# Kernel tuning notes

Hardware: AMD Instinct MI355X
Metric: run time of the kernel (lower is better)

Reference implementation:

```python
import jax, jax.numpy as jnp
import numpy as np

H = 16  # num_attention_heads

def setup_inputs() -> dict:
    key = jax.random.key(0)
    ks = jax.random.split(key, 4)
    B, S, D = 4, 2048, 1024
    scale = 1.0 / np.sqrt(D)
    return {
        "hidden_states": jax.random.normal(ks[0], (B, S, D), dtype=jnp.float32),
        "attention_mask": jnp.zeros((B, 1, 1, S), dtype=jnp.float32),
        "Wq": jax.random.normal(ks[1], (D, D), dtype=jnp.float32) * scale,
        "bq": jnp.zeros((D,), dtype=jnp.float32),
        "Wk": jax.random.normal(ks[2], (D, D), dtype=jnp.float32) * scale,
        "bk": jnp.zeros((D,), dtype=jnp.float32),
        "Wv": jax.random.normal(ks[3], (D, D), dtype=jnp.float32) * scale,
        "bv": jnp.zeros((D,), dtype=jnp.float32),
    }

def _split_heads(x, B, S):
    # [B,S,D] -> [B,H,S,Dh]
    return x.reshape(B, S, H, -1).transpose(0, 2, 1, 3)

def reference(hidden_states, attention_mask, Wq, bq, Wk, bk, Wv, bv):
    B, S, D = hidden_states.shape
    Dh = D // H
    q = _split_heads(hidden_states @ Wq.T + bq, B, S)  # [B,H,S,Dh]
    k = _split_heads(hidden_states @ Wk.T + bk, B, S)
    v = _split_heads(hidden_states @ Wv.T + bv, B, S)
    scores = jnp.einsum("bhqd,bhkd->bhqk", q, k) / jnp.sqrt(jnp.float32(Dh))
    scores = scores + attention_mask  # additive mask, broadcast [B,1,1,S]
    probs = jax.nn.softmax(scores, axis=-1)  # dropout is identity in eval mode
    ctx = jnp.einsum("bhqk,bhkd->bhqd", probs, v)  # [B,H,S,Dh]
    ctx = ctx.transpose(0, 2, 1, 3).reshape(B, S, D)
    return ctx
```

## Files before the change

kernel.cpp:

```cpp
#include <hip/hip_runtime.h>
#include <hip/hip_bf16.h>
#include <stdint.h>

#define LOG2E 1.44269504088896340736f
#define SCL   (0.125f * LOG2E)

typedef __attribute__((ext_vector_type(8)))  short short8;
typedef __attribute__((ext_vector_type(4)))  float floatx4;
typedef __attribute__((ext_vector_type(16))) float floatx16;
typedef __attribute__((ext_vector_type(4)))  unsigned short ushort4v;

#define GLP(g, l)                                                              \
    __builtin_amdgcn_global_load_lds(                                          \
        (const __attribute__((address_space(1))) void*)(g),                    \
        (__attribute__((address_space(3))) void*)(l), 16, 0, 0)

#if __has_builtin(__builtin_amdgcn_exp2f)
#define EXP2(x) __builtin_amdgcn_exp2f(x)
#else
#define EXP2(x) exp2f(x)
#endif

static __device__ __forceinline__ unsigned short f2bf(float f) {
    union { float f; unsigned u; } v; v.f = f;
    unsigned r = v.u + 0x7FFFu + ((v.u >> 16) & 1u);
    return (unsigned short)(r >> 16);
}

static __device__ __forceinline__ unsigned pack2bf(float a, float b) {
    __hip_bfloat162 h = __float22bfloat162_rn(make_float2(a, b));
    union { __hip_bfloat162 h; unsigned u; } c; c.h = h; return c.u;
}

__global__ __launch_bounds__(256) void cvt_kernel(const float* __restrict__ in,
                                                  unsigned short* __restrict__ out,
                                                  int n4) {
    int i = blockIdx.x * 256 + threadIdx.x;
    if (i < n4) {
        float4 v = ((const float4*)in)[i];
        ushort4v o;
        o.x = f2bf(v.x); o.y = f2bf(v.y); o.z = f2bf(v.z); o.w = f2bf(v.w);
        ((ushort4v*)out)[i] = o;
    }
}

__global__ __launch_bounds__(256) void cvt_w3m(const float* __restrict__ Wq,
                                               const float* __restrict__ Wk,
                                               const float* __restrict__ Wv,
                                               const float* __restrict__ mask,
                                               unsigned short* __restrict__ out,
                                               float* __restrict__ maskl) {
    int i = blockIdx.x * 256 + threadIdx.x;
    if (i < 786432) {
        const float* src; int j;
        if (i < 262144)      { src = Wq; j = i; }
        else if (i < 524288) { src = Wk; j = i - 262144; }
        else                 { src = Wv; j = i - 524288; }
        float4 v = ((const float4*)src)[j];
        ushort4v o;
        o.x = f2bf(v.x); o.y = f2bf(v.y); o.z = f2bf(v.z); o.w = f2bf(v.w);
        ((ushort4v*)out)[i] = o;
    } else if (i < 786432 + 2048) {
        int j = i - 786432;
        float4 v = ((const float4*)mask)[j];
        ((float4*)maskl)[j] = make_float4(v.x * LOG2E, v.y * LOG2E,
                                          v.z * LOG2E, v.w * LOG2E);
    }
}

__global__ __launch_bounds__(256) void qkv_gemm(
        const unsigned short* __restrict__ X,
        const unsigned short* __restrict__ W,
        const float* __restrict__ bq, const float* __restrict__ bk,
        const float* __restrict__ bv,
        unsigned short* __restrict__ Qf,
        unsigned short* __restrict__ Kf,
        unsigned short* __restrict__ Vt)
{
    __shared__ __align__(16) unsigned short sh[17408];
    unsigned short* Ash = sh;
    unsigned short* Bsh = sh + 8192;

    const int tid  = threadIdx.x;
    const int lane = tid & 63;
    const int wv   = tid >> 6;
    const int quad = lane >> 4;
    const int ln   = lane & 15;
    const int mBase = blockIdx.x * 128;
    const int nBase = blockIdx.y * 128;
    const int wm = (wv >> 1) * 64;
    const int wn = (wv & 1) * 64;

    floatx4 acc[4][4];
#pragma unroll
    for (int i = 0; i < 4; ++i)
#pragma unroll
        for (int j = 0; j < 4; ++j) acc[i][j] = 0.0f;

    const int sr = lane >> 3;
    const int kc = (lane & 7) ^ sr;

    for (int kb = 0; kb < 1024; kb += 64) {
        __syncthreads();
#pragma unroll
        for (int s = 0; s < 4; ++s) {
            const int seg = wv * 4 + s;
            const int row = seg * 8 + sr;
            GLP(X + (size_t)(mBase + row) * 1024 + kb + kc * 8, Ash + seg * 512);
            GLP(W + (size_t)(nBase + row) * 1024 + kb + kc * 8, Bsh + seg * 512);
        }
        __syncthreads();
#pragma unroll
        for (int kk = 0; kk < 2; ++kk) {
            const int c = kk * 4 + quad;
            short8 aF[4], bF[4];
#pragma unroll
            for (int i = 0; i < 4; ++i) {
                const int R = wm + i * 16 + ln;
                aF[i] = *(const short8*)(Ash + (R >> 3) * 512 + (R & 7) * 64 + ((c ^ (R & 7)) * 8));
            }
#pragma unroll
            for (int j = 0; j < 4; ++j) {
                const int R = wn + j * 16 + ln;
                bF[j] = *(const short8*)(Bsh + (R >> 3) * 512 + (R & 7) * 64 + ((c ^ (R & 7)) * 8));
            }
#pragma unroll
            for (int i = 0; i < 4; ++i)
#pragma unroll
                for (int j = 0; j < 4; ++j)
                    acc[i][j] = __builtin_amdgcn_mfma_f32_16x16x32_bf16(
                        aF[i], bF[j], acc[i][j], 0, 0, 0);
        }
    }

    if (blockIdx.y < 16) {
        unsigned short* dst = (blockIdx.y < 8) ? Qf : Kf;
        const float* bias   = (blockIdx.y < 8) ? bq : bk;
        const int nb = nBase & 1023;
        float bj[4];
#pragma unroll
        for (int j = 0; j < 4; ++j)
            bj[j] = bias[nb + wn + j * 16 + ln];
        __syncthreads();
#pragma unroll
        for (int j = 0; j < 4; ++j) {
            const int col = wn + j * 16 + ln;
#pragma unroll
            for (int i = 0; i < 4; ++i) {
                const int row0 = wm + i * 16 + quad * 4;
#pragma unroll
                for (int r = 0; r < 4; ++r)
                    sh[(row0 + r) * 136 + col] = f2bf(acc[i][j][r] + bj[j]);
            }
        }
        __syncthreads();
#pragma unroll
        for (int it = 0; it < 8; ++it) {
            const int row  = it * 16 + (tid >> 4);
            const int part = tid & 15;
            short8 v = *(const short8*)(sh + row * 136 + part * 8);
            *(short8*)(dst + (size_t)(mBase + row) * 1024 + nb + part * 8) = v;
        }
    } else {
#pragma unroll
        for (int j = 0; j < 4; ++j) {
            const int gn = nBase + wn + j * 16 + ln;
            const int c  = gn & 1023;
            const int h  = c >> 6;
            const int d  = c & 63;
            const float bias = bv[c];
#pragma unroll
            for (int i = 0; i < 4; ++i) {
                const int gm0 = mBase + wm + i * 16 + quad * 4;
                const int b   = gm0 >> 11;
                const int s0  = gm0 & 2047;
                ushort4v pv;
#pragma unroll
                for (int r = 0; r < 4; ++r) pv[r] = f2bf(acc[i][j][r] + bias);
                *(ushort4v*)(Vt + (size_t)((b * 16 + h) * 64 + d) * 2048 + s0) = pv;
            }
        }
    }
}

__global__ __launch_bounds__(256, 4) void attn_kernel(
        const unsigned short* __restrict__ Qf,
        const unsigned short* __restrict__ Kf,
        const unsigned short* __restrict__ VT,
        const float* __restrict__ maskl,
        float* __restrict__ out)
{
    __shared__ __align__(16) unsigned short Ksh[128 * 64];
    __shared__ __align__(16) unsigned short Vsh[64 * 128];
    __shared__ __align__(16) float Msh[128];
    __shared__ __align__(16) float Lsh[128];

    const int tid  = threadIdx.x;
    const int lane = tid & 63;
    const int wv   = tid >> 6;
    const int q32  = lane & 31;
    const int hi   = lane >> 5;
    const int bh   = blockIdx.x & 63;
    const int qt   = blockIdx.x >> 6;
    const int b    = bh >> 4;
    const int h    = bh & 15;
    const int q0   = qt * 128 + wv * 32;
    const int sw   = q32 & 7;

    short8 bQ[4];
#pragma unroll
    for (int ks = 0; ks < 4; ++ks)
        bQ[ks] = *(const short8*)(Qf + (size_t)(b * 2048 + q0 + q32) * 1024
                                     + h * 64 + ks * 16 + hi * 8);

    floatx16 accO0 = 0.0f, accO1 = 0.0f;
    float l_c = 0.0f;

    const unsigned short* gK = Kf + (size_t)(b * 2048) * 1024 + h * 64;
    const unsigned short* gV = VT + (size_t)(bh * 64) * 2048;
    const float* mrow = maskl + b * 2048;

    const int krr = lane >> 3;
    const int kcs = lane & 7;
    const int vrr = lane >> 4;
    const int vcs = lane & 15;

    for (int kb = 0; kb < 2048; kb += 128) {
        __syncthreads();
#pragma unroll
        for (int s = 0; s < 4; ++s) {
            const int seg = wv * 4 + s;
            const int rK  = seg * 8 + krr;
            const int cK  = kcs ^ (rK & 7);
            GLP(gK + (size_t)(kb + rK) * 1024 + cK * 8, Ksh + seg * 512);
            const int rV  = seg * 4 + vrr;
            const int cV  = vcs ^ (rV & 7);
            GLP(gV + (size_t)rV * 2048 + kb + cV * 8, Vsh + seg * 512);
        }
        if (tid < 32) GLP(mrow + kb + lane * 4, Msh);
        __syncthreads();

#pragma unroll
        for (int half = 0; half < 2; ++half) {
#pragma unroll
            for (int mt = 0; mt < 2; ++mt) {
                floatx16 sacc = 0.0f;
#pragma unroll
                for (int ks = 0; ks < 4; ++ks) {
                    const int row  = half * 64 + mt * 32 + q32;
                    const int slot = (2 * ks + hi) ^ sw;
                    short8 aK = *(const short8*)(Ksh + row * 64 + slot * 8);
                    sacc = __builtin_amdgcn_mfma_f32_32x32x16_bf16(aK, bQ[ks], sacc, 0, 0, 0);
                }
                unsigned u0[4], u1[4], e0[4], e1[4];
#pragma unroll
                for (int a = 0; a < 4; ++a) {
                    const int key0 = half * 64 + mt * 32 + a * 8 + hi * 4;
                    float4 mv4 = *(const float4*)(Msh + key0);
                    float p0 = EXP2(sacc[a * 4 + 0] * SCL + mv4.x);
                    float p1 = EXP2(sacc[a * 4 + 1] * SCL + mv4.y);
                    float p2 = EXP2(sacc[a * 4 + 2] * SCL + mv4.z);
                    float p3 = EXP2(sacc[a * 4 + 3] * SCL + mv4.w);
                    l_c += (p0 + p1) + (p2 + p3);
                    u0[a] = pack2bf(p0, p1);
                    u1[a] = pack2bf(p2, p3);
                    e0[a] = (unsigned)__shfl_xor((int)u0[a], 32, 64);
                    e1[a] = (unsigned)__shfl_xor((int)u1[a], 32, 64);
                }
#pragma unroll
                for (int ks2 = 0; ks2 < 2; ++ks2) {
                    const int a0 = ks2 * 2;
                    union { unsigned u[4]; short8 s; } aP;
                    aP.u[0] = hi ? e0[a0 + 1] : u0[a0];
                    aP.u[1] = hi ? e1[a0 + 1] : u1[a0];
                    aP.u[2] = hi ? u0[a0 + 1] : e0[a0];
                    aP.u[3] = hi ? u1[a0 + 1] : e1[a0];
                    const int ks = mt * 2 + ks2;
                    const int cv = half * 8 + ((2 * ks + hi) ^ sw);
                    short8 bV0 = *(const short8*)(Vsh + q32 * 128 + cv * 8);
                    short8 bV1 = *(const short8*)(Vsh + (32 + q32) * 128 + cv * 8);
                    accO0 = __builtin_amdgcn_mfma_f32_32x32x16_bf16(aP.s, bV0, accO0, 0, 0, 0);
                    accO1 = __builtin_amdgcn_mfma_f32_32x32x16_bf16(aP.s, bV1, accO1, 0, 0, 0);
                }
            }
        }
    }

    l_c += __shfl_xor(l_c, 32, 64);
    if (lane < 32) Lsh[wv * 32 + q32] = 1.0f / l_c;
#pragma unroll
    for (int g = 0; g < 4; ++g) {
        float4 inv4 = *(const float4*)(Lsh + wv * 32 + g * 8 + hi * 4);
#pragma unroll
        for (int rr = 0; rr < 4; ++rr) {
            const int r   = g * 4 + rr;
            const int row = rr + 8 * g + 4 * hi;
            const float linv = (rr == 0) ? inv4.x : (rr == 1) ? inv4.y
                             : (rr == 2) ? inv4.z : inv4.w;
            float* op = out + (size_t)(b * 2048 + q0 + row) * 1024 + h * 64 + q32;
            op[0]  = accO0[r] * linv;
            op[32] = accO1[r] * linv;
        }
    }
}

extern "C" void kernel_launch(void* const* d_in, const int* in_sizes, int n_in,
                              void* d_out, int out_size, void* d_ws, size_t ws_size,
                              hipStream_t stream) {
    const float* X    = (const float*)d_in[0];
    const float* mask = (const float*)d_in[1];
    const float* Wq   = (const float*)d_in[2];
    const float* bq   = (const float*)d_in[3];
    const float* Wk   = (const float*)d_in[4];
    const float* bk   = (const float*)d_in[5];
    const float* Wv   = (const float*)d_in[6];
    const float* bv   = (const float*)d_in[7];
    float* out = (float*)d_out;

    char* ws = (char*)d_ws;
    unsigned short* xb  = (unsigned short*)(ws);
    unsigned short* wb  = (unsigned short*)(ws + 16777216);
    unsigned short* qf  = (unsigned short*)(ws + 23068672);
    unsigned short* kf  = (unsigned short*)(ws + 39845888);
    unsigned short* vtb = (unsigned short*)(ws + 56623104);
    float*          ml  = (float*)(ws + 73400320);

    cvt_kernel<<<8192, 256, 0, stream>>>(X, xb, 2097152);
    cvt_w3m<<<3080, 256, 0, stream>>>(Wq, Wk, Wv, mask, wb, ml);

    qkv_gemm<<<dim3(64, 24), 256, 0, stream>>>(xb, wb, bq, bk, bv, qf, kf, vtb);

    attn_kernel<<<1024, 256, 0, stream>>>(qf, kf, vtb, ml, out);
}
```

Baseline: 263.1 us.

## Use 32x32 MFMA in QKV GEMM, fold softmax scale into Q, precompute LDS addresses

The projection GEMM now uses 32x32x16 bf16 MFMA with 2x2 accumulators per wave instead of 4x4 tiles of 16x16x32. This halves the LDS fragment loads per k-step. The softmax scale (including log2e) is folded into Q at the GEMM epilogue, and the mask is preloaded into the score accumulator, which removes the FMA before each exp2. LDS fragment pointers for K and V are hoisted out of the key loop. Scaling Q before the bf16 rounding changes rounding slightly.

New measurement: 262.2 us. About the same (-0.3%).

```diff
diff --git a/kernel.cpp b/kernel.cpp
--- a/kernel.cpp
+++ b/kernel.cpp
@@ -6,7 +6,6 @@
 #define SCL   (0.125f * LOG2E)
 
 typedef __attribute__((ext_vector_type(8)))  short short8;
-typedef __attribute__((ext_vector_type(4)))  float floatx4;
 typedef __attribute__((ext_vector_type(16))) float floatx16;
 typedef __attribute__((ext_vector_type(4)))  unsigned short ushort4v;
 
@@ -84,18 +83,15 @@
     const int tid  = threadIdx.x;
     const int lane = tid & 63;
     const int wv   = tid >> 6;
-    const int quad = lane >> 4;
-    const int ln   = lane & 15;
+    const int q32  = lane & 31;
+    const int hi   = lane >> 5;
     const int mBase = blockIdx.x * 128;
     const int nBase = blockIdx.y * 128;
     const int wm = (wv >> 1) * 64;
     const int wn = (wv & 1) * 64;
 
-    floatx4 acc[4][4];
-#pragma unroll
-    for (int i = 0; i < 4; ++i)
-#pragma unroll
-        for (int j = 0; j < 4; ++j) acc[i][j] = 0.0f;
+    floatx16 acc[2][2];
+    acc[0][0] = 0.0f; acc[0][1] = 0.0f; acc[1][0] = 0.0f; acc[1][1] = 0.0f;
 
     const int sr = lane >> 3;
     const int kc = (lane & 7) ^ sr;
@@ -111,47 +107,52 @@
         }
         __syncthreads();
 #pragma unroll
-        for (int kk = 0; kk < 2; ++kk) {
-            const int c = kk * 4 + quad;
-            short8 aF[4], bF[4];
-#pragma unroll
-            for (int i = 0; i < 4; ++i) {
-                const int R = wm + i * 16 + ln;
-                aF[i] = *(const short8*)(Ash + (R >> 3) * 512 + (R & 7) * 64 + ((c ^ (R & 7)) * 8));
+        for (int ks = 0; ks < 4; ++ks) {
+            short8 aF[2], bF[2];
+#pragma unroll
+            for (int mi = 0; mi < 2; ++mi) {
+                const int R = wm + mi * 32 + q32;
+                const int slot = (2 * ks + hi) ^ (R & 7);
+                aF[mi] = *(const short8*)(Ash + (R >> 3) * 512 + (R & 7) * 64 + slot * 8);
             }
 #pragma unroll
-            for (int j = 0; j < 4; ++j) {
-                const int R = wn + j * 16 + ln;
-                bF[j] = *(const short8*)(Bsh + (R >> 3) * 512 + (R & 7) * 64 + ((c ^ (R & 7)) * 8));
+            for (int ni = 0; ni < 2; ++ni) {
+                const int R = wn + ni * 32 + q32;
+                const int slot = (2 * ks + hi) ^ (R & 7);
+                bF[ni] = *(const short8*)(Bsh + (R >> 3) * 512 + (R & 7) * 64 + slot * 8);
             }
 #pragma unroll
-            for (int i = 0; i < 4; ++i)
-#pragma unroll
-                for (int j = 0; j < 4; ++j)
-                    acc[i][j] = __builtin_amdgcn_mfma_f32_16x16x32_bf16(
-                        aF[i], bF[j], acc[i][j], 0, 0, 0);
+            for (int mi = 0; mi < 2; ++mi)
+#pragma unroll
+                for (int ni = 0; ni < 2; ++ni)
+                    acc[mi][ni] = __builtin_amdgcn_mfma_f32_32x32x16_bf16(
+                        aF[mi], bF[ni], acc[mi][ni], 0, 0, 0);
         }
     }
 
     if (blockIdx.y < 16) {
         unsigned short* dst = (blockIdx.y < 8) ? Qf : Kf;
         const float* bias   = (blockIdx.y < 8) ? bq : bk;
+        const float scl     = (blockIdx.y < 8) ? SCL : 1.0f;
         const int nb = nBase & 1023;
-        float bj[4];
-#pragma unroll
-        for (int j = 0; j < 4; ++j)
-            bj[j] = bias[nb + wn + j * 16 + ln];
-        __syncthreads();
-#pragma unroll
-        for (int j = 0; j < 4; ++j) {
-            const int col = wn + j * 16 + ln;
-#pragma unroll
-            for (int i = 0; i < 4; ++i) {
-                const int row0 = wm + i * 16 + quad * 4;
-#pragma unroll
-                for (int r = 0; r < 4; ++r)
-                    sh[(row0 + r) * 136 + col] = f2bf(acc[i][j][r] + bj[j]);
-            }
+        float bj[2];
+#pragma unroll
+        for (int ni = 0; ni < 2; ++ni)
+            bj[ni] = bias[nb + wn + ni * 32 + q32];
+        __syncthreads();
+#pragma unroll
+        for (int ni = 0; ni < 2; ++ni) {
+            const int col = wn + ni * 32 + q32;
+#pragma unroll
+            for (int mi = 0; mi < 2; ++mi)
+#pragma unroll
+                for (int g = 0; g < 4; ++g) {
+                    const int row0 = wm + mi * 32 + g * 8 + hi * 4;
+#pragma unroll
+                    for (int rr = 0; rr < 4; ++rr)
+                        sh[(row0 + rr) * 136 + col] =
+                            f2bf((acc[mi][ni][g * 4 + rr] + bj[ni]) * scl);
+                }
         }
         __syncthreads();
 #pragma unroll
@@ -163,22 +164,25 @@
         }
     } else {
 #pragma unroll
-        for (int j = 0; j < 4; ++j) {
-            const int gn = nBase + wn + j * 16 + ln;
+        for (int ni = 0; ni < 2; ++ni) {
+            const int gn = nBase + wn + ni * 32 + q32;
             const int c  = gn & 1023;
             const int h  = c >> 6;
             const int d  = c & 63;
             const float bias = bv[c];
 #pragma unroll
-            for (int i = 0; i < 4; ++i) {
-                const int gm0 = mBase + wm + i * 16 + quad * 4;
-                const int b   = gm0 >> 11;
-                const int s0  = gm0 & 2047;
-                ushort4v pv;
-#pragma unroll
-                for (int r = 0; r < 4; ++r) pv[r] = f2bf(acc[i][j][r] + bias);
-                *(ushort4v*)(Vt + (size_t)((b * 16 + h) * 64 + d) * 2048 + s0) = pv;
-            }
+            for (int mi = 0; mi < 2; ++mi)
+#pragma unroll
+                for (int g = 0; g < 4; ++g) {
+                    const int m0 = mBase + wm + mi * 32 + g * 8 + hi * 4;
+                    const int b  = m0 >> 11;
+                    const int s0 = m0 & 2047;
+                    ushort4v pv;
+#pragma unroll
+                    for (int rr = 0; rr < 4; ++rr)
+                        pv[rr] = f2bf(acc[mi][ni][g * 4 + rr] + bias);
+                    *(ushort4v*)(Vt + (size_t)((b * 16 + h) * 64 + d) * 2048 + s0) = pv;
+                }
         }
     }
 }
@@ -220,6 +224,16 @@
     const unsigned short* gV = VT + (size_t)(bh * 64) * 2048;
     const float* mrow = maskl + b * 2048;
 
+    const unsigned short* kb4[4];
+    const unsigned short* vb4[4];
+#pragma unroll
+    for (int ks = 0; ks < 4; ++ks) {
+        const int cs = (2 * ks + hi) ^ sw;
+        kb4[ks] = Ksh + q32 * 64 + cs * 8;
+        vb4[ks] = Vsh + q32 * 128 + cs * 8;
+    }
+    const float* mbase = Msh + hi * 4;
+
     const int krr = lane >> 3;
     const int kcs = lane & 7;
     const int vrr = lane >> 4;
@@ -244,23 +258,25 @@
         for (int half = 0; half < 2; ++half) {
 #pragma unroll
             for (int mt = 0; mt < 2; ++mt) {
-                floatx16 sacc = 0.0f;
+                floatx16 sacc;
+#pragma unroll
+                for (int a = 0; a < 4; ++a) {
+                    float4 mv4 = *(const float4*)(mbase + half * 64 + mt * 32 + a * 8);
+                    sacc[a * 4 + 0] = mv4.x; sacc[a * 4 + 1] = mv4.y;
+                    sacc[a * 4 + 2] = mv4.z; sacc[a * 4 + 3] = mv4.w;
+                }
 #pragma unroll
                 for (int ks = 0; ks < 4; ++ks) {
-                    const int row  = half * 64 + mt * 32 + q32;
-                    const int slot = (2 * ks + hi) ^ sw;
-                    short8 aK = *(const short8*)(Ksh + row * 64 + slot * 8);
+                    short8 aK = *(const short8*)(kb4[ks] + half * 4096 + mt * 2048);
                     sacc = __builtin_amdgcn_mfma_f32_32x32x16_bf16(aK, bQ[ks], sacc, 0, 0, 0);
                 }
                 unsigned u0[4], u1[4], e0[4], e1[4];
 #pragma unroll
                 for (int a = 0; a < 4; ++a) {
-                    const int key0 = half * 64 + mt * 32 + a * 8 + hi * 4;
-                    float4 mv4 = *(const float4*)(Msh + key0);
-                    float p0 = EXP2(sacc[a * 4 + 0] * SCL + mv4.x);
-                    float p1 = EXP2(sacc[a * 4 + 1] * SCL + mv4.y);
-                    float p2 = EXP2(sacc[a * 4 + 2] * SCL + mv4.z);
-                    float p3 = EXP2(sacc[a * 4 + 3] * SCL + mv4.w);
+                    float p0 = EXP2(sacc[a * 4 + 0]);
+                    float p1 = EXP2(sacc[a * 4 + 1]);
+                    float p2 = EXP2(sacc[a * 4 + 2]);
+                    float p3 = EXP2(sacc[a * 4 + 3]);
                     l_c += (p0 + p1) + (p2 + p3);
                     u0[a] = pack2bf(p0, p1);
                     u1[a] = pack2bf(p2, p3);
@@ -276,9 +292,8 @@
                     aP.u[2] = hi ? u0[a0 + 1] : e0[a0];
                     aP.u[3] = hi ? u1[a0 + 1] : e1[a0];
                     const int ks = mt * 2 + ks2;
-                    const int cv = half * 8 + ((2 * ks + hi) ^ sw);
-                    short8 bV0 = *(const short8*)(Vsh + q32 * 128 + cv * 8);
-                    short8 bV1 = *(const short8*)(Vsh + (32 + q32) * 128 + cv * 8);
+                    short8 bV0 = *(const short8*)(vb4[ks] + half * 64);
+                    short8 bV1 = *(const short8*)(vb4[ks] + 4096 + half * 64);
                     accO0 = __builtin_amdgcn_mfma_f32_32x32x16_bf16(aP.s, bV0, accO0, 0, 0, 0);
                     accO1 = __builtin_amdgcn_mfma_f32_32x32x16_bf16(aP.s, bV1, accO1, 0, 0, 0);
                 }
```
